# Kernel tuning notes

Measured on AMD Instinct MI355X. Metric: run time of the kernel, lower is better.

## Reference

```python
import jax, jax.numpy as jnp
import numpy as np

B, I, O, C, U = 32, 2048, 32, 16, 32  # batch, in_channels(caps), out_capsules, in_capsules(dim), unit_size
NUM_ITERS = 3


def setup_inputs() -> dict:
    key = jax.random.key(0)
    k1, k2 = jax.random.split(key)
    x = jax.random.normal(k1, (B, I, C), dtype=jnp.float32)
    w = jax.random.normal(k2, (I, O, C, U), dtype=jnp.float32)
    return {"x": x, "w": w}


def _squash(v):
    # faithful to original: vec * |vec| / (1 + |vec|^2), norm over last (unit) dim
    n = jnp.linalg.norm(v, axis=-1, keepdims=True)
    return v * n / (1.0 + n * n)


def reference(x, w):
    # u_hat[b,i,o,u] = sum_c x[b,i,c] * w[i,o,c,u]   (the original's x @ w with singleton dims dropped)
    u_hat = jnp.einsum('bic,iocu->biou', x, w)  # [B,I,O,U]
    b_log = jnp.zeros((I, O, 1), dtype=x.dtype)
    v = None
    for _ in range(NUM_ITERS):
        # original computes softmax over dim=2 of [I,O,1] (a singleton dim) -> all ones; kept faithful
        c = jax.nn.softmax(b_log, axis=2)[..., 0]  # [I,O]
        s = jnp.einsum('io,biou->bou', c, u_hat)   # sum over input capsules
        v = _squash(s)                              # [B,O,U]
        # agreement: per-(b,i,o) dot(u_hat, v), then mean over batch (original's update.mean(dim=0))
        agree = jnp.einsum('biou,bou->io', u_hat, v) / B
        b_log = b_log + agree[..., None]
    return v[:, :, None, :]  # matches original v.squeeze(1) -> [B, O, 1, U]
```

## Files before the change

kernel.cpp:

```cpp
#include <hip/hip_runtime.h>
#include <math.h>

#define B_   32
#define I_   2048
#define O_   32
#define C_   16
#define U_   32
#define NCOL  (O_ * U_)
#define TI    8
#define NIG   (I_ / TI)
#define CQ    4
#define SLICE (B_ * NCOL)
#define XS    36


__global__ __launch_bounds__(512, 4) void caps_partial(const float* __restrict__ x,
                                                       const float* __restrict__ w,
                                                       float* __restrict__ ws) {
    __shared__ float xs[TI * C_ * XS];
    const int tid = threadIdx.x;
    const int ig  = blockIdx.x >> 2;
    const int cq  = blockIdx.x & 3;
    const int i0  = ig * TI;

    for (int k = tid; k < B_ * TI * C_; k += 512) {
        int b   = k >> 7;
        int rem = k & 127;
        xs[rem * XS + b] = x[(size_t)b * (I_ * C_) + (size_t)i0 * C_ + rem];
    }
    __syncthreads();

    const int colf4 = tid & 63;
    const int bg    = tid >> 6;
    const int o     = cq * 8 + (colf4 >> 3);
    const int u4    = (colf4 & 7) << 2;
    const float* wp = w + o * (C_ * U_) + u4;

    float4 acc[4];
#pragma unroll
    for (int b = 0; b < 4; ++b) acc[b] = make_float4(0.f, 0.f, 0.f, 0.f);

    for (int il = 0; il < TI; ++il) {
        const float* wpi = wp + (size_t)(i0 + il) * (O_ * C_ * U_);
        const float* xr  = &xs[il * C_ * XS + bg * 4];
#pragma unroll
        for (int cc = 0; cc < C_; cc += 8) {
            float4 wv[8];
#pragma unroll
            for (int j = 0; j < 8; ++j)
                wv[j] = *(const float4*)(wpi + (cc + j) * U_);
#pragma unroll
            for (int j = 0; j < 8; ++j) {
                float4 xq = *(const float4*)(xr + (cc + j) * XS);
                acc[0].x = fmaf(xq.x, wv[j].x, acc[0].x);
                acc[0].y = fmaf(xq.x, wv[j].y, acc[0].y);
                acc[0].z = fmaf(xq.x, wv[j].z, acc[0].z);
                acc[0].w = fmaf(xq.x, wv[j].w, acc[0].w);
                acc[1].x = fmaf(xq.y, wv[j].x, acc[1].x);
                acc[1].y = fmaf(xq.y, wv[j].y, acc[1].y);
                acc[1].z = fmaf(xq.y, wv[j].z, acc[1].z);
                acc[1].w = fmaf(xq.y, wv[j].w, acc[1].w);
                acc[2].x = fmaf(xq.z, wv[j].x, acc[2].x);
                acc[2].y = fmaf(xq.z, wv[j].y, acc[2].y);
                acc[2].z = fmaf(xq.z, wv[j].z, acc[2].z);
                acc[2].w = fmaf(xq.z, wv[j].w, acc[2].w);
                acc[3].x = fmaf(xq.w, wv[j].x, acc[3].x);
                acc[3].y = fmaf(xq.w, wv[j].y, acc[3].y);
                acc[3].z = fmaf(xq.w, wv[j].z, acc[3].z);
                acc[3].w = fmaf(xq.w, wv[j].w, acc[3].w);
            }
        }
    }

    float* op = ws + (size_t)ig * SLICE + (size_t)(bg * 4) * NCOL + cq * 256 + colf4 * 4;
#pragma unroll
    for (int b = 0; b < 4; ++b)
        *(float4*)(op + (size_t)b * NCOL) = acc[b];
}

__global__ __launch_bounds__(256) void caps_reduce_squash(const float* __restrict__ ws,
                                                          float* __restrict__ out) {
    __shared__ float sh[128];
    const int tl = threadIdx.x & 127;
    const int ph = threadIdx.x >> 7;
    const int t  = blockIdx.x * 128 + tl;
    const float* p = ws + (size_t)ph * (NIG / 2) * SLICE + t;
    float s = 0.f;
#pragma unroll 16
    for (int i = 0; i < NIG / 2; ++i)
        s += p[(size_t)i * SLICE];
    if (ph) sh[tl] = s;
    __syncthreads();
    if (ph == 0) {
        s += sh[tl];
        float ss = s * s;
        ss += __shfl_xor(ss, 1);
        ss += __shfl_xor(ss, 2);
        ss += __shfl_xor(ss, 4);
        ss += __shfl_xor(ss, 8);
        ss += __shfl_xor(ss, 16);
        float n = sqrtf(ss);
        out[t] = s * n / (1.0f + ss);
    }
}

__global__ __launch_bounds__(256, 2) void caps_main_atomic(const float* __restrict__ x,
                                                           const float* __restrict__ w,
                                                           float* __restrict__ out) {
    __shared__ float xsf[4 * C_ * 33];
    const int tid = threadIdx.x;
    const int i0 = blockIdx.x * 4;
    for (int k = tid; k < B_ * 4 * C_; k += 256) {
        int b = k >> 6, rem = k & 63;
        xsf[rem * 33 + b] = x[(size_t)b * (I_ * C_) + (size_t)i0 * C_ + rem];
    }
    __syncthreads();
    const int o = tid >> 3, u4 = (tid & 7) << 2;
    const float* wp = w + (size_t)i0 * (O_ * C_ * U_) + o * (C_ * U_) + u4;
    float4 acc[B_];
#pragma unroll
    for (int b = 0; b < B_; ++b) acc[b] = make_float4(0.f, 0.f, 0.f, 0.f);
    for (int il = 0; il < 4; ++il) {
        const float* wpi = wp + (size_t)il * (O_ * C_ * U_);
        const float* xr = &xsf[il * C_ * 33];
#pragma unroll
        for (int c = 0; c < C_; ++c) {
            float4 wv = *(const float4*)(wpi + c * U_);
            const float* xc = xr + c * 33;
#pragma unroll
            for (int b = 0; b < B_; ++b) {
                float xb = xc[b];
                acc[b].x = fmaf(xb, wv.x, acc[b].x);
                acc[b].y = fmaf(xb, wv.y, acc[b].y);
                acc[b].z = fmaf(xb, wv.z, acc[b].z);
                acc[b].w = fmaf(xb, wv.w, acc[b].w);
            }
        }
    }
    float* op = out + o * U_ + u4;
#pragma unroll
    for (int b = 0; b < B_; ++b) {
        float* p = op + (size_t)b * NCOL;
        atomicAdd(p + 0, acc[b].x);
        atomicAdd(p + 1, acc[b].y);
        atomicAdd(p + 2, acc[b].z);
        atomicAdd(p + 3, acc[b].w);
    }
}

__global__ void caps_squash_inplace(float* __restrict__ out) {
    int t = blockIdx.x * 256 + threadIdx.x;
    float s = out[t];
    float ss = s * s;
    ss += __shfl_xor(ss, 1);
    ss += __shfl_xor(ss, 2);
    ss += __shfl_xor(ss, 4);
    ss += __shfl_xor(ss, 8);
    ss += __shfl_xor(ss, 16);
    float n = sqrtf(ss);
    out[t] = s * n / (1.0f + ss);
}

extern "C" void kernel_launch(void* const* d_in, const int* in_sizes, int n_in,
                              void* d_out, int out_size, void* d_ws, size_t ws_size,
                              hipStream_t stream) {
    const float* x = (const float*)d_in[0];
    const float* w = (const float*)d_in[1];
    float* out = (float*)d_out;

    const size_t need = (size_t)NIG * SLICE * sizeof(float);
    if (ws_size >= need) {
        float* ws = (float*)d_ws;
        caps_partial<<<NIG * CQ, 512, 0, stream>>>(x, w, ws);
        caps_reduce_squash<<<SLICE / 128, 256, 0, stream>>>(ws, out);
    } else {
        hipMemsetAsync(out, 0, (size_t)SLICE * sizeof(float), stream);
        caps_main_atomic<<<I_ / 4, 256, 0, stream>>>(x, w, out);
        caps_squash_inplace<<<SLICE / 256, 256, 0, stream>>>(out);
    }
}
```

Before: 233.0 us.

## Double-buffer weight loads and halve partial-sum slices in caps kernels

Measured after the change: 375.9 us. 1.61x slower.

```diff
diff --git a/kernel.cpp b/kernel.cpp
--- a/kernel.cpp
+++ b/kernel.cpp
@@ -6,12 +6,13 @@
 #define O_   32
 #define C_   16
 #define U_   32
-#define NCOL  (O_ * U_)
-#define TI    8
-#define NIG   (I_ / TI)
-#define CQ    4
-#define SLICE (B_ * NCOL)
-#define XS    36
+#define NCOL   (O_ * U_)
+#define TI     16
+#define NIG    (I_ / TI)
+#define CQ     4
+#define SLICE  (B_ * NCOL)
+#define XS     36
+#define CHUNKS (TI * 2)
 
 
 __global__ __launch_bounds__(512, 4) void caps_partial(const float* __restrict__ x,
@@ -24,8 +25,8 @@
     const int i0  = ig * TI;
 
     for (int k = tid; k < B_ * TI * C_; k += 512) {
-        int b   = k >> 7;
-        int rem = k & 127;
+        int b   = k >> 8;
+        int rem = k & 255;
         xs[rem * XS + b] = x[(size_t)b * (I_ * C_) + (size_t)i0 * C_ + rem];
     }
     __syncthreads();
@@ -34,41 +35,53 @@
     const int bg    = tid >> 6;
     const int o     = cq * 8 + (colf4 >> 3);
     const int u4    = (colf4 & 7) << 2;
-    const float* wp = w + o * (C_ * U_) + u4;
+    const float* wp = w + (size_t)i0 * (O_ * C_ * U_) + o * (C_ * U_) + u4;
+    const float* xb = xs + bg * 4;
 
     float4 acc[4];
 #pragma unroll
     for (int b = 0; b < 4; ++b) acc[b] = make_float4(0.f, 0.f, 0.f, 0.f);
 
-    for (int il = 0; il < TI; ++il) {
-        const float* wpi = wp + (size_t)(i0 + il) * (O_ * C_ * U_);
-        const float* xr  = &xs[il * C_ * XS + bg * 4];
+    float4 wv[2][8];
 #pragma unroll
-        for (int cc = 0; cc < C_; cc += 8) {
-            float4 wv[8];
+    for (int j = 0; j < 8; ++j)
+        wv[0][j] = *(const float4*)(wp + j * U_);
+
+#pragma unroll 2
+    for (int k = 0; k < CHUNKS; ++k) {
+        const int cur = k & 1;
+        const int nxt = cur ^ 1;
+        if (k + 1 < CHUNKS) {
+            const int il1 = (k + 1) >> 1;
+            const int cc1 = ((k + 1) & 1) * 8;
+            const float* wpn = wp + (size_t)il1 * (O_ * C_ * U_) + cc1 * U_;
 #pragma unroll
             for (int j = 0; j < 8; ++j)
-                wv[j] = *(const float4*)(wpi + (cc + j) * U_);
+                wv[nxt][j] = *(const float4*)(wpn + j * U_);
+        }
+        const int il = k >> 1;
+        const int cc = (k & 1) * 8;
+        const float* xr = xb + (il * C_ + cc) * XS;
 #pragma unroll
-            for (int j = 0; j < 8; ++j) {
-                float4 xq = *(const float4*)(xr + (cc + j) * XS);
-                acc[0].x = fmaf(xq.x, wv[j].x, acc[0].x);
-                acc[0].y = fmaf(xq.x, wv[j].y, acc[0].y);
-                acc[0].z = fmaf(xq.x, wv[j].z, acc[0].z);
-                acc[0].w = fmaf(xq.x, wv[j].w, acc[0].w);
-                acc[1].x = fmaf(xq.y, wv[j].x, acc[1].x);
-                acc[1].y = fmaf(xq.y, wv[j].y, acc[1].y);
-                acc[1].z = fmaf(xq.y, wv[j].z, acc[1].z);
-                acc[1].w = fmaf(xq.y, wv[j].w, acc[1].w);
-                acc[2].x = fmaf(xq.z, wv[j].x, acc[2].x);
-                acc[2].y = fmaf(xq.z, wv[j].y, acc[2].y);
-                acc[2].z = fmaf(xq.z, wv[j].z, acc[2].z);
-                acc[2].w = fmaf(xq.z, wv[j].w, acc[2].w);
-                acc[3].x = fmaf(xq.w, wv[j].x, acc[3].x);
-                acc[3].y = fmaf(xq.w, wv[j].y, acc[3].y);
-                acc[3].z = fmaf(xq.w, wv[j].z, acc[3].z);
-                acc[3].w = fmaf(xq.w, wv[j].w, acc[3].w);
-            }
+        for (int j = 0; j < 8; ++j) {
+            float4 xq = *(const float4*)(xr + j * XS);
+            float4 wj = wv[cur][j];
+            acc[0].x = fmaf(xq.x, wj.x, acc[0].x);
+            acc[0].y = fmaf(xq.x, wj.y, acc[0].y);
+            acc[0].z = fmaf(xq.x, wj.z, acc[0].z);
+            acc[0].w = fmaf(xq.x, wj.w, acc[0].w);
+            acc[1].x = fmaf(xq.y, wj.x, acc[1].x);
+            acc[1].y = fmaf(xq.y, wj.y, acc[1].y);
+            acc[1].z = fmaf(xq.y, wj.z, acc[1].z);
+            acc[1].w = fmaf(xq.y, wj.w, acc[1].w);
+            acc[2].x = fmaf(xq.z, wj.x, acc[2].x);
+            acc[2].y = fmaf(xq.z, wj.y, acc[2].y);
+            acc[2].z = fmaf(xq.z, wj.z, acc[2].z);
+            acc[2].w = fmaf(xq.z, wj.w, acc[2].w);
+            acc[3].x = fmaf(xq.w, wj.x, acc[3].x);
+            acc[3].y = fmaf(xq.w, wj.y, acc[3].y);
+            acc[3].z = fmaf(xq.w, wj.z, acc[3].z);
+            acc[3].w = fmaf(xq.w, wj.w, acc[3].w);
         }
     }
 
@@ -80,19 +93,20 @@
 
 __global__ __launch_bounds__(256) void caps_reduce_squash(const float* __restrict__ ws,
                                                           float* __restrict__ out) {
-    __shared__ float sh[128];
-    const int tl = threadIdx.x & 127;
-    const int ph = threadIdx.x >> 7;
-    const int t  = blockIdx.x * 128 + tl;
-    const float* p = ws + (size_t)ph * (NIG / 2) * SLICE + t;
+    __shared__ float sh[256];
+    const int tid = threadIdx.x;
+    const int tl = tid & 63;
+    const int ph = tid >> 6;
+    const int t  = blockIdx.x * 64 + tl;
+    const float* p = ws + (size_t)ph * (NIG / 4) * SLICE + t;
     float s = 0.f;
-#pragma unroll 16
-    for (int i = 0; i < NIG / 2; ++i)
+#pragma unroll 8
+    for (int i = 0; i < NIG / 4; ++i)
         s += p[(size_t)i * SLICE];
-    if (ph) sh[tl] = s;
+    sh[tid] = s;
     __syncthreads();
     if (ph == 0) {
-        s += sh[tl];
+        s = sh[tl] + sh[64 + tl] + sh[128 + tl] + sh[192 + tl];
         float ss = s * s;
         ss += __shfl_xor(ss, 1);
         ss += __shfl_xor(ss, 2);
@@ -172,7 +186,7 @@
     if (ws_size >= need) {
         float* ws = (float*)d_ws;
         caps_partial<<<NIG * CQ, 512, 0, stream>>>(x, w, ws);
-        caps_reduce_squash<<<SLICE / 128, 256, 0, stream>>>(ws, out);
+        caps_reduce_squash<<<SLICE / 64, 256, 0, stream>>>(ws, out);
     } else {
         hipMemsetAsync(out, 0, (size_t)SLICE * sizeof(float), stream);
         caps_main_atomic<<<I_ / 4, 256, 0, stream>>>(x, w, out);
```
